# Performance work log

Hardware: AMD Instinct MI355X
Metric: run time of the kernel (lower is better)

Reference implementation:

```python
import jax, jax.numpy as jnp
import numpy as np

B, L, C = 64, 2688, 256
W, S, H = 42, 21, 8   # window_size, shift_size, num_heads
HD = C // H
NW = L // W
MLP_H = 4 * C


def _layer_norm(v, g, b, eps=1e-5):
    m = v.mean(-1, keepdims=True)
    var = ((v - m) ** 2).mean(-1, keepdims=True)
    return (v - m) / jnp.sqrt(var + eps) * g + b


def setup_inputs() -> dict:
    key = jax.random.key(0)
    ks = jax.random.split(key, 8)
    std = 0.02
    return {
        "x": jax.random.normal(ks[0], (B, L, C), jnp.float32),
        "norm1_g": jnp.ones((C,), jnp.float32),
        "norm1_b": jnp.zeros((C,), jnp.float32),
        "qkv_w": jax.random.normal(ks[1], (C, 3 * C), jnp.float32) * std,
        "qkv_b": jnp.zeros((3 * C,), jnp.float32),
        "bias_table": jax.random.normal(ks[2], (2 * W - 1, H), jnp.float32) * std,
        "proj_w": jax.random.normal(ks[3], (C, C), jnp.float32) * std,
        "proj_b": jnp.zeros((C,), jnp.float32),
        "norm2_g": jnp.ones((C,), jnp.float32),
        "norm2_b": jnp.zeros((C,), jnp.float32),
        "fc1_w": jax.random.normal(ks[4], (C, MLP_H), jnp.float32) * std,
        "fc1_b": jnp.zeros((MLP_H,), jnp.float32),
        "fc2_w": jax.random.normal(ks[5], (MLP_H, C), jnp.float32) * std,
        "fc2_b": jnp.zeros((C,), jnp.float32),
    }


# ---- static (data-independent) index/mask tables ----
_rel_idx = np.arange(W)[None, :] - np.arange(W)[:, None] + W - 1  # (W, W)
_seg = np.zeros((L,), np.float32)
_seg[-W:-S] = 1.0
_seg[-S:] = 2.0
_mw = _seg.reshape(NW, W)
_am = _mw[:, None, :] - _mw[:, :, None]            # (nW, W, W)
_ATTN_MASK = np.where(_am != 0, -100.0, 0.0).astype(np.float32)


def reference(x, norm1_g, norm1_b, qkv_w, qkv_b, bias_table, proj_w, proj_b,
              norm2_g, norm2_b, fc1_w, fc1_b, fc2_w, fc2_b):
    mask = jnp.asarray(_ATTN_MASK)                  # (nW, W, W)
    scale = HD ** -0.5

    shortcut = x
    h = _layer_norm(x, norm1_g, norm1_b)
    h = jnp.roll(h, -S, axis=1)                     # cyclic shift
    xw = h.reshape(B * NW, W, C)                    # window partition

    qkv = (xw @ qkv_w + qkv_b).reshape(B * NW, W, 3, H, HD).transpose(2, 0, 3, 1, 4)
    q, k, v = qkv[0] * scale, qkv[1], qkv[2]        # each (B_, H, W, HD)
    attn = jnp.einsum('bhnd,bhmd->bhnm', q, k)      # (B_, H, W, W)

    rpb = bias_table[jnp.asarray(_rel_idx)]         # (W, W, H)
    attn = attn + rpb.transpose(2, 0, 1)[None]
    attn = attn.reshape(B, NW, H, W, W) + mask[None, :, None]
    attn = jax.nn.softmax(attn.reshape(B * NW, H, W, W), axis=-1)

    o = jnp.einsum('bhnm,bhmd->bhnd', attn, v)      # (B_, H, W, HD)
    o = o.transpose(0, 2, 1, 3).reshape(B * NW, W, C)
    o = o @ proj_w + proj_b

    h = jnp.roll(o.reshape(B, L, C), S, axis=1)     # reverse shift
    x1 = shortcut + h

    m = _layer_norm(x1, norm2_g, norm2_b)
    m = jax.nn.gelu(m @ fc1_w + fc1_b, approximate=False)
    m = m @ fc2_w + fc2_b
    return x1 + m
```

## Files before the change

### kernel.cpp

```cpp
#include <hip/hip_runtime.h>
#include <hip/hip_bf16.h>

typedef short short8 __attribute__((ext_vector_type(8)));
typedef float floatx4 __attribute__((ext_vector_type(4)));

constexpr int Bc = 64, Lc = 2688, Cc = 256, Wc = 42, Sc = 21;
constexpr int Mrows = Bc * Lc;
constexpr float QSCALE = 0.17677669529663689f;

#define GLOAD_LDS(g, l) __builtin_amdgcn_global_load_lds( \
    (const __attribute__((address_space(1))) void*)(g),   \
    (__attribute__((address_space(3))) void*)(l), 16, 0, 0)

__global__ __launch_bounds__(256) void transpose_cast_k(const float* __restrict__ w,
                                                        __hip_bfloat16* __restrict__ o,
                                                        int K, int N) {
  __shared__ float tile[32][33];
  int tx = threadIdx.x & 31, ty = threadIdx.x >> 5;
  int n0 = blockIdx.x * 32, k0 = blockIdx.y * 32;
#pragma unroll
  for (int r = 0; r < 32; r += 8)
    tile[ty + r][tx] = w[(size_t)(k0 + ty + r) * N + n0 + tx];
  __syncthreads();
#pragma unroll
  for (int r = 0; r < 32; r += 8)
    o[(size_t)(n0 + ty + r) * K + k0 + tx] = __float2bfloat16(tile[tx][ty + r]);
}

__global__ __launch_bounds__(256) void ln_k(const float* __restrict__ x, const float* __restrict__ g,
                                            const float* __restrict__ bta, __hip_bfloat16* __restrict__ out,
                                            int roll) {
  int row = blockIdx.x * 4 + (threadIdx.x >> 6);
  int lane = threadIdx.x & 63;
  int bb = row / Lc, rl = row - bb * Lc;
  int sl = rl + roll; if (sl >= Lc) sl -= Lc;
  const float4 v = *(const float4*)(x + ((size_t)bb * Lc + sl) * Cc + lane * 4);
  float s = v.x + v.y + v.z + v.w;
#pragma unroll
  for (int o = 1; o < 64; o <<= 1) s += __shfl_xor(s, o, 64);
  float mean = s * (1.0f / Cc);
  float d0 = v.x - mean, d1 = v.y - mean, d2 = v.z - mean, d3 = v.w - mean;
  float s2 = d0 * d0 + d1 * d1 + d2 * d2 + d3 * d3;
#pragma unroll
  for (int o = 1; o < 64; o <<= 1) s2 += __shfl_xor(s2, o, 64);
  float r = rsqrtf(s2 * (1.0f / Cc) + 1e-5f);
  const float4 gg = *(const float4*)(g + lane * 4);
  const float4 bb4 = *(const float4*)(bta + lane * 4);
  __hip_bfloat16 tmp[4];
  tmp[0] = __float2bfloat16(d0 * r * gg.x + bb4.x);
  tmp[1] = __float2bfloat16(d1 * r * gg.y + bb4.y);
  tmp[2] = __float2bfloat16(d2 * r * gg.z + bb4.z);
  tmp[3] = __float2bfloat16(d3 * r * gg.w + bb4.w);
  *(uint2*)(out + (size_t)row * Cc + lane * 4) = *(uint2*)tmp;
}

template <int EPI>
__global__ __launch_bounds__(256) void gemm_bt(const __hip_bfloat16* __restrict__ A,
                                               const __hip_bfloat16* __restrict__ BT,
                                               const float* __restrict__ bias,
                                               const float* __restrict__ aux,
                                               void* __restrict__ outv,
                                               int N, int K) {
  const int n0 = blockIdx.x * 128, m0 = blockIdx.y * 128;
  __shared__ __align__(16) __hip_bfloat16 As[128 * 32];
  __shared__ __align__(16) __hip_bfloat16 Bs[128 * 32];
  const int t = threadIdx.x;
  const int wave = t >> 6, lane = t & 63, q = lane >> 4, lr = lane & 15;
  const int wm = (wave >> 1) * 64, wn = (wave & 1) * 64;

  const int srow = t >> 2, sk = (t & 3) * 8;
  const __hip_bfloat16* gA0 = A + (size_t)(m0 + srow) * K + sk;
  const __hip_bfloat16* gA1 = gA0 + (size_t)64 * K;
  const __hip_bfloat16* gB0 = BT + (size_t)(n0 + srow) * K + sk;
  const __hip_bfloat16* gB1 = gB0 + (size_t)64 * K;
  __hip_bfloat16* lA0 = As + wave * 512;
  __hip_bfloat16* lA1 = As + 2048 + wave * 512;
  __hip_bfloat16* lB0 = Bs + wave * 512;
  __hip_bfloat16* lB1 = Bs + 2048 + wave * 512;

  floatx4 acc[4][4] = {};
  for (int k0 = 0; k0 < K; k0 += 32) {
    GLOAD_LDS(gA0 + k0, lA0);
    GLOAD_LDS(gA1 + k0, lA1);
    GLOAD_LDS(gB0 + k0, lB0);
    GLOAD_LDS(gB1 + k0, lB1);
    __syncthreads();
    short8 af[4], bf[4];
#pragma unroll
    for (int i = 0; i < 4; i++) af[i] = *(const short8*)(As + (wm + i * 16 + lr) * 32 + q * 8);
#pragma unroll
    for (int j = 0; j < 4; j++) bf[j] = *(const short8*)(Bs + (wn + j * 16 + lr) * 32 + q * 8);
#pragma unroll
    for (int i = 0; i < 4; i++)
#pragma unroll
      for (int j = 0; j < 4; j++)
        acc[i][j] = __builtin_amdgcn_mfma_f32_16x16x32_bf16(af[i], bf[j], acc[i][j], 0, 0, 0);
    __syncthreads();
  }
#pragma unroll
  for (int i = 0; i < 4; i++) {
#pragma unroll
    for (int rg = 0; rg < 4; rg++) {
      int row = m0 + wm + i * 16 + q * 4 + rg;
      int bb = 0, l = 0;
      if (EPI == 1) {
        bb = row / Lc;
        int rl = row - bb * Lc;
        l = rl + Sc; if (l >= Lc) l -= Lc;
      }
#pragma unroll
      for (int j = 0; j < 4; j++) {
        int col = n0 + wn + j * 16 + lr;
        float v = acc[i][j][rg] + bias[col];
        if (EPI == 0) {
          if (col < 256) v *= QSCALE;
          ((__hip_bfloat16*)outv)[(size_t)row * N + col] = __float2bfloat16(v);
        } else if (EPI == 1) {
          size_t o = ((size_t)bb * Lc + l) * Cc + col;
          ((float*)outv)[o] = aux[o] + v;
        } else if (EPI == 2) {
          v = 0.5f * v * (1.0f + erff(v * 0.70710678118654752f));
          ((__hip_bfloat16*)outv)[(size_t)row * N + col] = __float2bfloat16(v);
        } else {
          size_t o = (size_t)row * Cc + col;
          ((float*)outv)[o] = aux[o] + v;
        }
      }
    }
  }
}

constexpr int PSTR = 72;
constexpr int PSZ = 48 * PSTR;
constexpr int VTSZ = 32 * PSTR;

__global__ __launch_bounds__(256) void attn_k(const __hip_bfloat16* __restrict__ qkv,
                                              const float* __restrict__ bias_table,
                                              __hip_bfloat16* __restrict__ o_buf) {
  __shared__ __align__(16) __hip_bfloat16 smem[4 * PSZ + 4 * VTSZ];
  __shared__ float btab[83 * 8];
  const int t = threadIdx.x, wave = t >> 6, lane = t & 63, q = lane >> 4, lr = lane & 15;
  const int win = blockIdx.x >> 1;
  const int h = (blockIdx.x & 1) * 4 + wave;

  for (int i = t; i < (4 * PSZ + 4 * VTSZ) / 8; i += 256) ((uint4*)smem)[i] = uint4{0, 0, 0, 0};
  for (int i = t; i < 83 * 8; i += 256) btab[i] = bias_table[i];
  __syncthreads();

  __hip_bfloat16* Pw = smem + wave * PSZ;
  __hip_bfloat16* VTw = smem + 4 * PSZ + wave * VTSZ;
  const __hip_bfloat16* qbase = qkv + (size_t)win * 42 * 768 + h * 32;
  const __hip_bfloat16* kbase = qbase + 256;
  const __hip_bfloat16* vbase = qbase + 512;

  for (int c = lane; c < 42 * 4; c += 64) {
    int j = c >> 2, d0 = (c & 3) * 8;
    short8 vv = *(const short8*)(vbase + (size_t)j * 768 + d0);
#pragma unroll
    for (int e = 0; e < 8; e++) ((short*)VTw)[(d0 + e) * PSTR + j] = vv[e];
  }

  short8 qf[3], kf[3];
#pragma unroll
  for (int mt = 0; mt < 3; mt++) {
    int i = mt * 16 + lr; if (i > 41) i = 41;
    qf[mt] = *(const short8*)(qbase + (size_t)i * 768 + q * 8);
  }
#pragma unroll
  for (int nt = 0; nt < 3; nt++) {
    int j = nt * 16 + lr; if (j > 41) j = 41;
    kf[nt] = *(const short8*)(kbase + (size_t)j * 768 + q * 8);
  }
  floatx4 sacc[3][3] = {};
#pragma unroll
  for (int mt = 0; mt < 3; mt++)
#pragma unroll
    for (int nt = 0; nt < 3; nt++)
      sacc[mt][nt] = __builtin_amdgcn_mfma_f32_16x16x32_bf16(qf[mt], kf[nt], sacc[mt][nt], 0, 0, 0);

  const bool lastwin = ((win & 63) == 63);
#pragma unroll
  for (int mt = 0; mt < 3; mt++) {
#pragma unroll
    for (int rg = 0; rg < 4; rg++) {
      int row = mt * 16 + q * 4 + rg;
      float sv[3];
      float mx = -1e30f;
#pragma unroll
      for (int nt = 0; nt < 3; nt++) {
        int col = nt * 16 + lr;
        float s = sacc[mt][nt][rg];
        int ri = col - row + 41; ri = ri < 0 ? 0 : (ri > 82 ? 82 : ri);
        s += btab[ri * 8 + h];
        if (lastwin && ((row < 21) != (col < 21))) s -= 100.0f;
        if (col >= 42) s = -1e30f;
        sv[nt] = s;
        mx = fmaxf(mx, s);
      }
#pragma unroll
      for (int o = 1; o < 16; o <<= 1) mx = fmaxf(mx, __shfl_xor(mx, o, 64));
      float sum = 0.0f;
#pragma unroll
      for (int nt = 0; nt < 3; nt++) { float e = __expf(sv[nt] - mx); sv[nt] = e; sum += e; }
#pragma unroll
      for (int o = 1; o < 16; o <<= 1) sum += __shfl_xor(sum, o, 64);
      float inv = 1.0f / sum;
#pragma unroll
      for (int nt = 0; nt < 3; nt++) Pw[row * PSTR + nt * 16 + lr] = __float2bfloat16(sv[nt] * inv);
    }
  }
  __syncthreads();

  floatx4 oacc[3][2] = {};
#pragma unroll
  for (int ks = 0; ks < 2; ks++) {
    short8 pf[3], vf[2];
#pragma unroll
    for (int mt = 0; mt < 3; mt++) pf[mt] = *(const short8*)(Pw + (mt * 16 + lr) * PSTR + ks * 32 + q * 8);
#pragma unroll
    for (int nt = 0; nt < 2; nt++) vf[nt] = *(const short8*)(VTw + (nt * 16 + lr) * PSTR + ks * 32 + q * 8);
#pragma unroll
    for (int mt = 0; mt < 3; mt++)
#pragma unroll
      for (int nt = 0; nt < 2; nt++)
        oacc[mt][nt] = __builtin_amdgcn_mfma_f32_16x16x32_bf16(pf[mt], vf[nt], oacc[mt][nt], 0, 0, 0);
  }
#pragma unroll
  for (int mt = 0; mt < 3; mt++) {
#pragma unroll
    for (int rg = 0; rg < 4; rg++) {
      int row = mt * 16 + q * 4 + rg;
      if (row < 42) {
#pragma unroll
        for (int nt = 0; nt < 2; nt++) {
          int col = nt * 16 + lr;
          o_buf[((size_t)win * 42 + row) * 256 + h * 32 + col] = __float2bfloat16(oacc[mt][nt][rg]);
        }
      }
    }
  }
}

extern "C" void kernel_launch(void* const* d_in, const int* in_sizes, int n_in,
                              void* d_out, int out_size, void* d_ws, size_t ws_size,
                              hipStream_t stream) {
  const float* x       = (const float*)d_in[0];
  const float* norm1_g = (const float*)d_in[1];
  const float* norm1_b = (const float*)d_in[2];
  const float* qkv_w   = (const float*)d_in[3];
  const float* qkv_b   = (const float*)d_in[4];
  const float* btab    = (const float*)d_in[5];
  const float* proj_w  = (const float*)d_in[6];
  const float* proj_b  = (const float*)d_in[7];
  const float* norm2_g = (const float*)d_in[8];
  const float* norm2_b = (const float*)d_in[9];
  const float* fc1_w   = (const float*)d_in[10];
  const float* fc1_b   = (const float*)d_in[11];
  const float* fc2_w   = (const float*)d_in[12];
  const float* fc2_b   = (const float*)d_in[13];
  float* out = (float*)d_out;

  char* ws = (char*)d_ws;
  size_t off = 0;
  auto alloc = [&](size_t bytes) { char* p = ws + off; off += (bytes + 255) & ~(size_t)255; return p; };
  __hip_bfloat16* wT_qkv  = (__hip_bfloat16*)alloc((size_t)768 * 256 * 2);
  __hip_bfloat16* wT_proj = (__hip_bfloat16*)alloc((size_t)256 * 256 * 2);
  __hip_bfloat16* wT_fc1  = (__hip_bfloat16*)alloc((size_t)1024 * 256 * 2);
  __hip_bfloat16* wT_fc2  = (__hip_bfloat16*)alloc((size_t)256 * 1024 * 2);
  __hip_bfloat16* buf88   = (__hip_bfloat16*)alloc((size_t)Mrows * 256 * 2);
  __hip_bfloat16* buf352  = (__hip_bfloat16*)alloc((size_t)Mrows * 1024 * 2);

  transpose_cast_k<<<dim3(768 / 32, 256 / 32), 256, 0, stream>>>(qkv_w, wT_qkv, 256, 768);
  transpose_cast_k<<<dim3(256 / 32, 256 / 32), 256, 0, stream>>>(proj_w, wT_proj, 256, 256);
  transpose_cast_k<<<dim3(1024 / 32, 256 / 32), 256, 0, stream>>>(fc1_w, wT_fc1, 256, 1024);
  transpose_cast_k<<<dim3(256 / 32, 1024 / 32), 256, 0, stream>>>(fc2_w, wT_fc2, 1024, 256);

  ln_k<<<Mrows / 4, 256, 0, stream>>>(x, norm1_g, norm1_b, buf88, Sc);

  gemm_bt<0><<<dim3(768 / 128, Mrows / 128), 256, 0, stream>>>(buf88, wT_qkv, qkv_b, nullptr, buf352, 768, 256);

  attn_k<<<(Mrows / Wc) * 2, 256, 0, stream>>>(buf352, btab, buf88);

  gemm_bt<1><<<dim3(256 / 128, Mrows / 128), 256, 0, stream>>>(buf88, wT_proj, proj_b, x, out, 256, 256);

  ln_k<<<Mrows / 4, 256, 0, stream>>>(out, norm2_g, norm2_b, buf88, 0);

  gemm_bt<2><<<dim3(1024 / 128, Mrows / 128), 256, 0, stream>>>(buf88, wT_fc1, fc1_b, nullptr, buf352, 1024, 256);

  gemm_bt<3><<<dim3(256 / 128, Mrows / 128), 256, 0, stream>>>(buf352, wT_fc2, fc2_b, out, out, 256, 1024);

  (void)in_sizes; (void)n_in; (void)out_size; (void)ws_size;
}
```

Measured before the change: 1.163 ms.

## Replace GEMM with 256x256 tile, double-buffered, swizzled LDS, 8-wave kernel

Swaps the simple 128x128 single-buffered bf16 GEMM for a 512-thread kernel with 256x256 tiles and a K step of 64. Global-to-LDS loads are double-buffered and interleaved with MFMA phases using explicit waitcnt, barriers and setprio. The LDS layout uses an XOR swizzle to avoid bank conflicts, and workgroup IDs are remapped across XCDs for better L2 locality. It uses 128KB of LDS per block and a large accumulator set, which can limit occupancy, and the hand-written waitcnt sequencing is fragile.

After: 1.144 ms. About the same (-1.7%).

```diff
diff --git a/kernel.cpp b/kernel.cpp
--- a/kernel.cpp
+++ b/kernel.cpp
@@ -11,6 +11,11 @@
 #define GLOAD_LDS(g, l) __builtin_amdgcn_global_load_lds( \
     (const __attribute__((address_space(1))) void*)(g),   \
     (__attribute__((address_space(3))) void*)(l), 16, 0, 0)
+#define BAR() __builtin_amdgcn_s_barrier()
+#define WAITV4() asm volatile("s_waitcnt vmcnt(4)" ::: "memory")
+#define WAITV0() asm volatile("s_waitcnt vmcnt(0)" ::: "memory")
+#define LGKM0() do { asm volatile("s_waitcnt lgkmcnt(0)" ::: "memory"); \
+                     __builtin_amdgcn_sched_barrier(0); } while (0)
 
 __global__ __launch_bounds__(256) void transpose_cast_k(const float* __restrict__ w,
                                                         __hip_bfloat16* __restrict__ o,
@@ -54,54 +59,122 @@
   *(uint2*)(out + (size_t)row * Cc + lane * 4) = *(uint2*)tmp;
 }
 
-template <int EPI>
-__global__ __launch_bounds__(256) void gemm_bt(const __hip_bfloat16* __restrict__ A,
-                                               const __hip_bfloat16* __restrict__ BT,
-                                               const float* __restrict__ bias,
-                                               const float* __restrict__ aux,
-                                               void* __restrict__ outv,
-                                               int N, int K) {
-  const int n0 = blockIdx.x * 128, m0 = blockIdx.y * 128;
-  __shared__ __align__(16) __hip_bfloat16 As[128 * 32];
-  __shared__ __align__(16) __hip_bfloat16 Bs[128 * 32];
+template <int EPI, int N, int K>
+__global__ __launch_bounds__(512, 2) void gemm8(const __hip_bfloat16* __restrict__ A,
+                                                const __hip_bfloat16* __restrict__ BT,
+                                                const float* __restrict__ bias,
+                                                const float* __restrict__ aux,
+                                                void* __restrict__ outv) {
+  constexpr int NT = K / 64;
+  constexpr int NBX = N / 256;
+  constexpr int NWG = NBX * (Mrows / 256);
+  static_assert(NWG % 8 == 0, "xcd swizzle");
+  __shared__ __align__(16) __hip_bfloat16 As[32768];
+  __shared__ __align__(16) __hip_bfloat16 Bs[32768];
+
   const int t = threadIdx.x;
   const int wave = t >> 6, lane = t & 63, q = lane >> 4, lr = lane & 15;
-  const int wm = (wave >> 1) * 64, wn = (wave & 1) * 64;
-
-  const int srow = t >> 2, sk = (t & 3) * 8;
-  const __hip_bfloat16* gA0 = A + (size_t)(m0 + srow) * K + sk;
-  const __hip_bfloat16* gA1 = gA0 + (size_t)64 * K;
-  const __hip_bfloat16* gB0 = BT + (size_t)(n0 + srow) * K + sk;
-  const __hip_bfloat16* gB1 = gB0 + (size_t)64 * K;
-  __hip_bfloat16* lA0 = As + wave * 512;
-  __hip_bfloat16* lA1 = As + 2048 + wave * 512;
-  __hip_bfloat16* lB0 = Bs + wave * 512;
-  __hip_bfloat16* lB1 = Bs + 2048 + wave * 512;
-
-  floatx4 acc[4][4] = {};
-  for (int k0 = 0; k0 < K; k0 += 32) {
-    GLOAD_LDS(gA0 + k0, lA0);
-    GLOAD_LDS(gA1 + k0, lA1);
-    GLOAD_LDS(gB0 + k0, lB0);
-    GLOAD_LDS(gB1 + k0, lB1);
-    __syncthreads();
-    short8 af[4], bf[4];
-#pragma unroll
-    for (int i = 0; i < 4; i++) af[i] = *(const short8*)(As + (wm + i * 16 + lr) * 32 + q * 8);
-#pragma unroll
-    for (int j = 0; j < 4; j++) bf[j] = *(const short8*)(Bs + (wn + j * 16 + lr) * 32 + q * 8);
-#pragma unroll
-    for (int i = 0; i < 4; i++)
-#pragma unroll
-      for (int j = 0; j < 4; j++)
-        acc[i][j] = __builtin_amdgcn_mfma_f32_16x16x32_bf16(af[i], bf[j], acc[i][j], 0, 0, 0);
-    __syncthreads();
-  }
-#pragma unroll
-  for (int i = 0; i < 4; i++) {
+  const int wm = (wave >> 2) * 128, wn = (wave & 3) * 64;
+
+  const int orig = blockIdx.x;
+  const int wgid = (orig & 7) * (NWG / 8) + (orig >> 3);
+  const int bx = wgid % NBX, by = wgid / NBX;
+  const int n0 = bx * 256, m0 = by * 256;
+
+  auto srcoff = [&](int c) {
+    int o = c * 16;
+    int u = o ^ (((o >> 8) & 3) << 4);
+    return (size_t)(u >> 6) * K + (size_t)((u >> 4) & 3) * 8;
+  };
+  const __hip_bfloat16* sA0 = A + (size_t)m0 * K + srcoff(t);
+  const __hip_bfloat16* sA1 = A + (size_t)m0 * K + srcoff(512 + t);
+  const __hip_bfloat16* sB0 = BT + (size_t)n0 * K + srcoff(t);
+  const __hip_bfloat16* sB1 = BT + (size_t)n0 * K + srcoff(512 + t);
+
+  int offA[8], offB[4];
+#pragma unroll
+  for (int i = 0; i < 8; i++) {
+    int lin = (wm + i * 16 + lr) * 64 + q * 16;
+    offA[i] = lin ^ (((lin >> 8) & 3) << 4);
+  }
+#pragma unroll
+  for (int j = 0; j < 4; j++) {
+    int lin = (wn + j * 16 + lr) * 64 + q * 16;
+    offB[j] = lin ^ (((lin >> 8) & 3) << 4);
+  }
+
+  floatx4 acc[8][4] = {};
+  short8 afr[4], bfr[4];
+
+#define STAGE(s0, s1, region, koff) do {            \
+    __hip_bfloat16* l_ = (region) + wave * 512;     \
+    GLOAD_LDS((s0) + (koff), l_);                   \
+    GLOAD_LDS((s1) + (koff), l_ + 4096); } while (0)
+
+#define LDA4(base_, mq_) { \
+    const char* Ab_ = (const char*)(base_); \
+    _Pragma("unroll") for (int i_ = 0; i_ < 4; i_++) afr[i_] = *(const short8*)(Ab_ + offA[(mq_) * 4 + i_]); }
+#define LDB4(base_) { \
+    const char* Bb_ = (const char*)(base_); \
+    _Pragma("unroll") for (int j_ = 0; j_ < 4; j_++) bfr[j_] = *(const short8*)(Bb_ + offB[j_]); }
+#define MFMA16(mq_) \
+    __builtin_amdgcn_s_setprio(1); \
+    _Pragma("unroll") for (int i_ = 0; i_ < 4; i_++) \
+    _Pragma("unroll") for (int j_ = 0; j_ < 4; j_++) \
+      acc[(mq_) * 4 + i_][j_] = __builtin_amdgcn_mfma_f32_16x16x32_bf16(afr[i_], bfr[j_], acc[(mq_) * 4 + i_][j_], 0, 0, 0); \
+    __builtin_amdgcn_s_setprio(0);
+
+  STAGE(sA0, sA1, As + 0 * 8192, 0);
+  STAGE(sB0, sB1, Bs + 0 * 8192, 0);
+  STAGE(sA0, sA1, As + 1 * 8192, 32);
+  STAGE(sB0, sB1, Bs + 1 * 8192, 32);
+  WAITV0();
+  BAR();
+
+  for (int kt = 0; kt < NT - 1; ++kt) {
+    const int buf = kt & 1, nbuf = buf ^ 1;
+    const int kn = (kt + 1) * 64;
+    __hip_bfloat16* A0 = As + (buf * 2 + 0) * 8192;
+    __hip_bfloat16* A1 = As + (buf * 2 + 1) * 8192;
+    __hip_bfloat16* B0 = Bs + (buf * 2 + 0) * 8192;
+    __hip_bfloat16* B1 = Bs + (buf * 2 + 1) * 8192;
+    LDA4(A0, 0); LDB4(B0);
+    STAGE(sA0, sA1, As + (nbuf * 2 + 0) * 8192, kn);
+    BAR(); LGKM0(); MFMA16(0); BAR();
+    LDA4(A0, 1);
+    STAGE(sB0, sB1, Bs + (nbuf * 2 + 0) * 8192, kn);
+    BAR(); LGKM0(); MFMA16(1);
+    WAITV4(); BAR();
+    LDA4(A1, 0); LDB4(B1);
+    STAGE(sA0, sA1, As + (nbuf * 2 + 1) * 8192, kn + 32);
+    BAR(); LGKM0(); MFMA16(0); BAR();
+    LDA4(A1, 1);
+    STAGE(sB0, sB1, Bs + (nbuf * 2 + 1) * 8192, kn + 32);
+    BAR(); LGKM0(); MFMA16(1);
+    WAITV4(); BAR();
+  }
+  {
+    const int buf = (NT - 1) & 1;
+    __hip_bfloat16* A0 = As + (buf * 2 + 0) * 8192;
+    __hip_bfloat16* A1 = As + (buf * 2 + 1) * 8192;
+    __hip_bfloat16* B0 = Bs + (buf * 2 + 0) * 8192;
+    __hip_bfloat16* B1 = Bs + (buf * 2 + 1) * 8192;
+    LDA4(A0, 0); LDB4(B0);
+    BAR(); LGKM0(); MFMA16(0); BAR();
+    LDA4(A0, 1);
+    BAR(); LGKM0(); MFMA16(1);
+    WAITV0(); BAR();
+    LDA4(A1, 0); LDB4(B1);
+    BAR(); LGKM0(); MFMA16(0); BAR();
+    LDA4(A1, 1);
+    LGKM0(); MFMA16(1);
+  }
+
+#pragma unroll
+  for (int mf = 0; mf < 8; mf++) {
 #pragma unroll
     for (int rg = 0; rg < 4; rg++) {
-      int row = m0 + wm + i * 16 + q * 4 + rg;
+      int row = m0 + wm + mf * 16 + q * 4 + rg;
       int bb = 0, l = 0;
       if (EPI == 1) {
         bb = row / Lc;
@@ -109,9 +182,9 @@
         l = rl + Sc; if (l >= Lc) l -= Lc;
       }
 #pragma unroll
-      for (int j = 0; j < 4; j++) {
-        int col = n0 + wn + j * 16 + lr;
-        float v = acc[i][j][rg] + bias[col];
+      for (int nf = 0; nf < 4; nf++) {
+        int col = n0 + wn + nf * 16 + lr;
+        float v = acc[mf][nf][rg] + bias[col];
         if (EPI == 0) {
           if (col < 256) v *= QSCALE;
           ((__hip_bfloat16*)outv)[(size_t)row * N + col] = __float2bfloat16(v);
@@ -128,6 +201,10 @@
       }
     }
   }
+#undef STAGE
+#undef LDA4
+#undef LDB4
+#undef MFMA16
 }
 
 constexpr int PSTR = 72;
@@ -277,17 +354,17 @@
 
   ln_k<<<Mrows / 4, 256, 0, stream>>>(x, norm1_g, norm1_b, buf88, Sc);
 
-  gemm_bt<0><<<dim3(768 / 128, Mrows / 128), 256, 0, stream>>>(buf88, wT_qkv, qkv_b, nullptr, buf352, 768, 256);
+  gemm8<0, 768, 256><<<dim3(3 * (Mrows / 256)), 512, 0, stream>>>(buf88, wT_qkv, qkv_b, nullptr, buf352);
 
   attn_k<<<(Mrows / Wc) * 2, 256, 0, stream>>>(buf352, btab, buf88);
 
-  gemm_bt<1><<<dim3(256 / 128, Mrows / 128), 256, 0, stream>>>(buf88, wT_proj, proj_b, x, out, 256, 256);
+  gemm8<1, 256, 256><<<dim3(Mrows / 256), 512, 0, stream>>>(buf88, wT_proj, proj_b, x, out);
 
   ln_k<<<Mrows / 4, 256, 0, stream>>>(out, norm2_g, norm2_b, buf88, 0);
 
-  gemm_bt<2><<<dim3(1024 / 128, Mrows / 128), 256, 0, stream>>>(buf88, wT_fc1, fc1_b, nullptr, buf352, 1024, 256);
-
-  gemm_bt<3><<<dim3(256 / 128, Mrows / 128), 256, 0, stream>>>(buf352, wT_fc2, fc2_b, out, out, 256, 1024);
+  gemm8<2, 1024, 256><<<dim3(4 * (Mrows / 256)), 512, 0, stream>>>(buf88, wT_fc1, fc1_b, nullptr, buf352);
+
+  gemm8<3, 256, 1024><<<dim3(Mrows / 256), 512, 0, stream>>>(buf352, wT_fc2, fc2_b, out, out);
 
   (void)in_sizes; (void)n_in; (void)out_size; (void)ws_size;
 }
```
